# Kernel optimization log

Hardware: AMD Instinct MI355X
Metric: run time of the kernel (lower is better)

## Reference

```python
import jax, jax.numpy as jnp
import numpy as np

N_NODES = 50000
N_EDGES = 800000
NDIM_IN = 64
EDIM = 64
NDIM_OUT = [128, 128]


def setup_inputs() -> dict:
    key = jax.random.key(0)
    ks = jax.random.split(key, 12)
    inp = {
        "nfeats": jax.random.normal(ks[0], (N_NODES, 1, NDIM_IN), dtype=jnp.float32),
        "efeats": jax.random.normal(ks[1], (N_EDGES, 1, EDIM), dtype=jnp.float32),
        "dst": jax.random.randint(ks[2], (N_EDGES,), 0, N_NODES, dtype=jnp.int32),
    }
    # Layer 0 MLP: Linear(ndim_in+edim -> 128), ReLU, Linear(128 -> 128), ReLU
    d0_in = NDIM_IN + EDIM
    s = 1.0 / np.sqrt(d0_in)
    inp["W1_0"] = jax.random.uniform(ks[3], (d0_in, NDIM_OUT[0]), jnp.float32, -s, s)
    inp["b1_0"] = jax.random.uniform(ks[4], (NDIM_OUT[0],), jnp.float32, -s, s)
    s = 1.0 / np.sqrt(NDIM_OUT[0])
    inp["W2_0"] = jax.random.uniform(ks[5], (NDIM_OUT[0], NDIM_OUT[0]), jnp.float32, -s, s)
    inp["b2_0"] = jax.random.uniform(ks[6], (NDIM_OUT[0],), jnp.float32, -s, s)
    # Layer 1 MLP: Linear(128+edim -> 128), ReLU, Linear(128 -> 128), ReLU
    d1_in = NDIM_OUT[0] + EDIM
    s = 1.0 / np.sqrt(d1_in)
    inp["W1_1"] = jax.random.uniform(ks[7], (d1_in, NDIM_OUT[1]), jnp.float32, -s, s)
    inp["b1_1"] = jax.random.uniform(ks[8], (NDIM_OUT[1],), jnp.float32, -s, s)
    s = 1.0 / np.sqrt(NDIM_OUT[1])
    inp["W2_1"] = jax.random.uniform(ks[9], (NDIM_OUT[1], NDIM_OUT[1]), jnp.float32, -s, s)
    inp["b2_1"] = jax.random.uniform(ks[10], (NDIM_OUT[1],), jnp.float32, -s, s)
    return inp


def _gin_layer(h, h_neigh, W1, b1, W2, b2):
    # concat node state with scatter-summed edge features, then 2-layer MLP
    x = jnp.concatenate([h, h_neigh], axis=-1)  # [N, 1, d_in + edim]
    x = jax.nn.relu(x @ W1 + b1)
    return jax.nn.relu(x @ W2 + b2)


def reference(nfeats, efeats, dst,
              W1_0, b1_0, W2_0, b2_0,
              W1_1, b1_1, W2_1, b2_1):
    n = nfeats.shape[0]
    # update_all(copy_e, sum): scatter-add edge features onto destination nodes.
    # efeats never changes (edge_update path disabled), so h_neigh is layer-invariant.
    h_neigh = jax.ops.segment_sum(efeats, dst, num_segments=n)  # [N, 1, edim]
    h = _gin_layer(nfeats, h_neigh, W1_0, b1_0, W2_0, b2_0)
    # dropout is identity in eval mode (deterministic reference)
    h = _gin_layer(h, h_neigh, W1_1, b1_1, W2_1, b2_1)
    return h.sum(axis=1)  # [N, ndim_out[-1]]
```

## Files before the change

kernel.cpp:

```cpp
#include <hip/hip_runtime.h>
#include <hip/hip_bf16.h>

#define N_NODES 50000
#define N_EDGES 800000
#define EDIM 64
#define NT 64
#define XS 200
#define N_TILES 49

typedef __attribute__((ext_vector_type(8))) short  bf16x8_t;
typedef __attribute__((ext_vector_type(4))) short  bf16x4_t;
typedef __attribute__((ext_vector_type(4))) float  f32x4_t;

__device__ __forceinline__ unsigned short f2bf(float f) {
    unsigned u = __float_as_uint(f);
    unsigned r = u + 0x7fff + ((u >> 16) & 1);
    return (unsigned short)(r >> 16);
}
__device__ __forceinline__ float bf2f(unsigned short s) {
    return __uint_as_float(((unsigned)s) << 16);
}

__global__ __launch_bounds__(256) void prep_w_kernel(
    const float* __restrict__ W1_0, const float* __restrict__ W2_0,
    const float* __restrict__ W1_1, const float* __restrict__ W2_1,
    unsigned short* __restrict__ wbuf)
{
    int bid = blockIdx.x, t = threadIdx.x;
    const float* W; unsigned short *whi, *wlo; int K, idx;
    if (bid < 64)       { W = W1_0; K = 128; whi = wbuf;          wlo = wbuf + 16384;  idx = bid * 256 + t; }
    else if (bid < 128) { W = W2_0; K = 128; whi = wbuf + 32768;  wlo = wbuf + 49152;  idx = (bid - 64) * 256 + t; }
    else if (bid < 224) { W = W1_1; K = 192; whi = wbuf + 65536;  wlo = wbuf + 90112;  idx = (bid - 128) * 256 + t; }
    else                { W = W2_1; K = 128; whi = wbuf + 114688; wlo = wbuf + 131072; idx = (bid - 224) * 256 + t; }
    int k = idx >> 7, n = idx & 127;
    float w = W[idx];
    unsigned short h = f2bf(w);
    unsigned short l = f2bf(w - bf2f(h));
    whi[n * K + k] = h;
    wlo[n * K + k] = l;
}


__global__ __launch_bounds__(256) void hist_kernel(const int* __restrict__ dst,
                                                   int* __restrict__ cnt)
{
    int i = blockIdx.x * 256 + threadIdx.x;
    if (i < N_EDGES / 4) {
        int4 d = ((const int4*)dst)[i];
        atomicAdd(&cnt[d.x], 1);
        atomicAdd(&cnt[d.y], 1);
        atomicAdd(&cnt[d.z], 1);
        atomicAdd(&cnt[d.w], 1);
    }
}

__global__ __launch_bounds__(1024) void scan_reduce_kernel(const int* __restrict__ cnt,
                                                           int* __restrict__ btot)
{
    __shared__ int wsum[16];
    int t = threadIdx.x, lane = t & 63, w = t >> 6;
    int i = blockIdx.x * 1024 + t;
    int v = (i < N_NODES) ? cnt[i] : 0;
    #pragma unroll
    for (int off = 32; off > 0; off >>= 1) v += __shfl_xor(v, off);
    if (lane == 0) wsum[w] = v;
    __syncthreads();
    if (w == 0) {
        int s = (lane < 16) ? wsum[lane] : 0;
        #pragma unroll
        for (int off = 32; off > 0; off >>= 1) s += __shfl_xor(s, off);
        if (lane == 0) btot[blockIdx.x] = s;
    }
}

__global__ __launch_bounds__(1024) void scan_apply_kernel(int* __restrict__ cnt,
                                                          const int* __restrict__ btot)
{
    __shared__ int wsum[16];
    __shared__ int base_s;
    int t = threadIdx.x, lane = t & 63, w = t >> 6;

    if (t < 64) {
        int v = (t < N_TILES) ? btot[t] : 0;
        int x = v;
        #pragma unroll
        for (int off = 1; off < 64; off <<= 1) {
            int u = __shfl_up(x, off);
            if (lane >= off) x += u;
        }
        if (t == blockIdx.x) base_s = x - v;
    }

    int i = blockIdx.x * 1024 + t;
    int v = (i < N_NODES) ? cnt[i] : 0;
    int x = v;
    #pragma unroll
    for (int off = 1; off < 64; off <<= 1) {
        int u = __shfl_up(x, off);
        if (lane >= off) x += u;
    }
    if (lane == 63) wsum[w] = x;
    __syncthreads();
    if (w == 0) {
        int s = (lane < 16) ? wsum[lane] : 0;
        #pragma unroll
        for (int off = 1; off < 16; off <<= 1) {
            int u = __shfl_up(s, off);
            if (lane >= off) s += u;
        }
        if (lane < 16) wsum[lane] = s;
    }
    __syncthreads();
    int base = base_s + ((w == 0) ? 0 : wsum[w - 1]);
    if (i < N_NODES) cnt[i] = base + (x - v);
}

__global__ __launch_bounds__(256) void reorder_kernel(const int* __restrict__ dst,
                                                      int* __restrict__ offs,
                                                      int* __restrict__ order)
{
    int i = blockIdx.x * 256 + threadIdx.x;
    if (i < N_EDGES / 4) {
        int4 d = ((const int4*)dst)[i];
        int e0 = i * 4;
        int p0 = atomicAdd(&offs[d.x], 1);
        int p1 = atomicAdd(&offs[d.y], 1);
        int p2 = atomicAdd(&offs[d.z], 1);
        int p3 = atomicAdd(&offs[d.w], 1);
        order[p0] = e0;
        order[p1] = e0 + 1;
        order[p2] = e0 + 2;
        order[p3] = e0 + 3;
    }
}

__global__ __launch_bounds__(256) void gather_kernel(const float* __restrict__ ef,
                                                     const int* __restrict__ offs,
                                                     const int* __restrict__ order,
                                                     float* __restrict__ hn)
{
    int node = blockIdx.x * 4 + (threadIdx.x >> 6);
    int lane = threadIdx.x & 63;
    if (node >= N_NODES) return;
    int s = (node == 0) ? 0 : offs[node - 1];
    int e = offs[node];
    float a[8];
    #pragma unroll
    for (int k = 0; k < 8; ++k) a[k] = 0.f;

    int j = s;
    for (; j + 8 <= e; j += 8) {
        int idx[8];
        #pragma unroll
        for (int k = 0; k < 8; ++k) idx[k] = order[j + k];
        #pragma unroll
        for (int k = 0; k < 8; ++k)
            a[k] += __builtin_nontemporal_load(ef + (size_t)idx[k] * 64 + lane);
    }
    for (; j < e; ++j)
        a[0] += __builtin_nontemporal_load(ef + (size_t)order[j] * 64 + lane);

    float r = ((a[0] + a[1]) + (a[2] + a[3])) + ((a[4] + a[5]) + (a[6] + a[7]));
    hn[(size_t)node * 64 + lane] = r;
}


__device__ __forceinline__ void stage_x(short* Xhi, short* Xlo,
                                        const float* __restrict__ g,
                                        int node0, int k0, int t)
{
    #pragma unroll
    for (int rep = 0; rep < 4; ++rep) {
        int idx  = rep * 256 + t;
        int node = idx >> 4;
        int kq   = idx & 15;
        int gn   = node0 + node;
        float4 v = make_float4(0.f, 0.f, 0.f, 0.f);
        if (gn < N_NODES) v = *(const float4*)(g + (size_t)gn * 64 + kq * 4);
        unsigned short h0 = f2bf(v.x), h1 = f2bf(v.y), h2 = f2bf(v.z), h3 = f2bf(v.w);
        bf16x4_t hv = {(short)h0, (short)h1, (short)h2, (short)h3};
        bf16x4_t lv = {(short)f2bf(v.x - bf2f(h0)), (short)f2bf(v.y - bf2f(h1)),
                       (short)f2bf(v.z - bf2f(h2)), (short)f2bf(v.w - bf2f(h3))};
        *(bf16x4_t*)(&Xhi[node * XS + k0 + kq * 4]) = hv;
        *(bf16x4_t*)(&Xlo[node * XS + k0 + kq * 4]) = lv;
    }
}

template <int KTOT, bool FINAL>
__device__ __forceinline__ void mfma_linear(short* Xhi, short* Xlo,
    const unsigned short* __restrict__ whi, const unsigned short* __restrict__ wlo,
    const float* __restrict__ bias, float* __restrict__ out, int node0, int t)
{
    const int lane = t & 63, wv = t >> 6, quad = lane >> 4, l15 = lane & 15;
    const int chb = wv * 32;

    f32x4_t acc[4][2];
    #pragma unroll
    for (int mt = 0; mt < 4; ++mt) {
        acc[mt][0] = (f32x4_t){0.f, 0.f, 0.f, 0.f};
        acc[mt][1] = (f32x4_t){0.f, 0.f, 0.f, 0.f};
    }
    float bv0 = bias[chb + l15];
    float bv1 = bias[chb + 16 + l15];

    const unsigned short* w0h = whi + (size_t)(chb + l15) * KTOT;
    const unsigned short* w0l = wlo + (size_t)(chb + l15) * KTOT;
    const unsigned short* w1h = whi + (size_t)(chb + 16 + l15) * KTOT;
    const unsigned short* w1l = wlo + (size_t)(chb + 16 + l15) * KTOT;

    #pragma unroll
    for (int ks = 0; ks < KTOT / 32; ++ks) {
        int kk = ks * 32 + quad * 8;
        bf16x8_t b0h = *(const bf16x8_t*)(w0h + kk);
        bf16x8_t b0l = *(const bf16x8_t*)(w0l + kk);
        bf16x8_t b1h = *(const bf16x8_t*)(w1h + kk);
        bf16x8_t b1l = *(const bf16x8_t*)(w1l + kk);
        #pragma unroll
        for (int mt = 0; mt < 4; ++mt) {
            bf16x8_t ah = *(const bf16x8_t*)(&Xhi[(mt * 16 + l15) * XS + kk]);
            bf16x8_t al = *(const bf16x8_t*)(&Xlo[(mt * 16 + l15) * XS + kk]);
            acc[mt][0] = __builtin_amdgcn_mfma_f32_16x16x32_bf16(ah, b0h, acc[mt][0], 0, 0, 0);
            acc[mt][0] = __builtin_amdgcn_mfma_f32_16x16x32_bf16(al, b0h, acc[mt][0], 0, 0, 0);
            acc[mt][0] = __builtin_amdgcn_mfma_f32_16x16x32_bf16(ah, b0l, acc[mt][0], 0, 0, 0);
            acc[mt][1] = __builtin_amdgcn_mfma_f32_16x16x32_bf16(ah, b1h, acc[mt][1], 0, 0, 0);
            acc[mt][1] = __builtin_amdgcn_mfma_f32_16x16x32_bf16(al, b1h, acc[mt][1], 0, 0, 0);
            acc[mt][1] = __builtin_amdgcn_mfma_f32_16x16x32_bf16(ah, b1l, acc[mt][1], 0, 0, 0);
        }
    }

    __syncthreads();

    if (!FINAL) {
        #pragma unroll
        for (int mt = 0; mt < 4; ++mt) {
            #pragma unroll
            for (int nt = 0; nt < 2; ++nt) {
                float bb = nt ? bv1 : bv0;
                int ch = chb + nt * 16 + l15;
                #pragma unroll
                for (int r = 0; r < 4; ++r) {
                    float y = fmaxf(acc[mt][nt][r] + bb, 0.f);
                    unsigned short h = f2bf(y);
                    unsigned short l = f2bf(y - bf2f(h));
                    int m = mt * 16 + quad * 4 + r;
                    Xhi[m * XS + ch] = (short)h;
                    Xlo[m * XS + ch] = (short)l;
                }
            }
        }
        __syncthreads();
    } else {
        #pragma unroll
        for (int mt = 0; mt < 4; ++mt) {
            #pragma unroll
            for (int nt = 0; nt < 2; ++nt) {
                float bb = nt ? bv1 : bv0;
                int ch = chb + nt * 16 + l15;
                #pragma unroll
                for (int r = 0; r < 4; ++r) {
                    int gn = node0 + mt * 16 + quad * 4 + r;
                    if (gn < N_NODES)
                        out[(size_t)gn * 128 + ch] = fmaxf(acc[mt][nt][r] + bb, 0.f);
                }
            }
        }
    }
}

__global__ __launch_bounds__(256) void gin_mlp_mfma_kernel(
    const float* __restrict__ nfeats, const float* __restrict__ hneigh,
    const unsigned short* __restrict__ wbuf,
    const float* __restrict__ b1_0, const float* __restrict__ b2_0,
    const float* __restrict__ b1_1, const float* __restrict__ b2_1,
    float* __restrict__ out)
{
    __shared__ short Xhi[NT * XS];
    __shared__ short Xlo[NT * XS];
    const int t = threadIdx.x;
    const int node0 = blockIdx.x * NT;

    stage_x(Xhi, Xlo, nfeats, node0, 0, t);
    stage_x(Xhi, Xlo, hneigh, node0, 64, t);
    stage_x(Xhi, Xlo, hneigh, node0, 128, t);
    __syncthreads();

    mfma_linear<128, false>(Xhi, Xlo, wbuf,          wbuf + 16384,  b1_0, nullptr, node0, t);
    mfma_linear<128, false>(Xhi, Xlo, wbuf + 32768,  wbuf + 49152,  b2_0, nullptr, node0, t);
    mfma_linear<192, false>(Xhi, Xlo, wbuf + 65536,  wbuf + 90112,  b1_1, nullptr, node0, t);
    mfma_linear<128, true >(Xhi, Xlo, wbuf + 114688, wbuf + 131072, b2_1, out,     node0, t);
}

extern "C" void kernel_launch(void* const* d_in, const int* in_sizes, int n_in,
                              void* d_out, int out_size, void* d_ws, size_t ws_size,
                              hipStream_t stream)
{
    const float* nfeats = (const float*)d_in[0];
    const float* efeats = (const float*)d_in[1];
    const int*   dst    = (const int*)d_in[2];
    const float* W1_0   = (const float*)d_in[3];
    const float* b1_0   = (const float*)d_in[4];
    const float* W2_0   = (const float*)d_in[5];
    const float* b2_0   = (const float*)d_in[6];
    const float* W1_1   = (const float*)d_in[7];
    const float* b1_1   = (const float*)d_in[8];
    const float* W2_1   = (const float*)d_in[9];
    const float* b2_1   = (const float*)d_in[10];
    float* out = (float*)d_out;

    char* ws = (char*)d_ws;
    float*          hneigh = (float*)ws;
    int*            offs   = (int*)(ws + 12800000);
    int*            order  = (int*)(ws + 13000192);
    int*            btot   = (int*)(ws + 16200192);
    unsigned short* wbuf   = (unsigned short*)(ws + 16200448);

    hipMemsetAsync(offs, 0, N_NODES * sizeof(int), stream);

    prep_w_kernel<<<288, 256, 0, stream>>>(W1_0, W2_0, W1_1, W2_1, wbuf);

    hist_kernel<<<(N_EDGES / 4 + 255) / 256, 256, 0, stream>>>(dst, offs);
    scan_reduce_kernel<<<N_TILES, 1024, 0, stream>>>(offs, btot);
    scan_apply_kernel<<<N_TILES, 1024, 0, stream>>>(offs, btot);
    reorder_kernel<<<(N_EDGES / 4 + 255) / 256, 256, 0, stream>>>(dst, offs, order);
    gather_kernel<<<(N_NODES + 3) / 4, 256, 0, stream>>>(efeats, offs, order, hneigh);

    int nblk = (N_NODES + NT - 1) / NT;
    gin_mlp_mfma_kernel<<<nblk, 256, 0, stream>>>(
        nfeats, hneigh, wbuf, b1_0, b2_0, b1_1, b2_1, out);
}
```

Measured before the change: 451.1 us.

## Fuse edge-feature gather into the MLP kernel, writing sums directly to LDS

```diff
diff --git a/kernel.cpp b/kernel.cpp
--- a/kernel.cpp
+++ b/kernel.cpp
@@ -132,36 +132,6 @@
         order[p2] = e0 + 2;
         order[p3] = e0 + 3;
     }
-}
-
-__global__ __launch_bounds__(256) void gather_kernel(const float* __restrict__ ef,
-                                                     const int* __restrict__ offs,
-                                                     const int* __restrict__ order,
-                                                     float* __restrict__ hn)
-{
-    int node = blockIdx.x * 4 + (threadIdx.x >> 6);
-    int lane = threadIdx.x & 63;
-    if (node >= N_NODES) return;
-    int s = (node == 0) ? 0 : offs[node - 1];
-    int e = offs[node];
-    float a[8];
-    #pragma unroll
-    for (int k = 0; k < 8; ++k) a[k] = 0.f;
-
-    int j = s;
-    for (; j + 8 <= e; j += 8) {
-        int idx[8];
-        #pragma unroll
-        for (int k = 0; k < 8; ++k) idx[k] = order[j + k];
-        #pragma unroll
-        for (int k = 0; k < 8; ++k)
-            a[k] += __builtin_nontemporal_load(ef + (size_t)idx[k] * 64 + lane);
-    }
-    for (; j < e; ++j)
-        a[0] += __builtin_nontemporal_load(ef + (size_t)order[j] * 64 + lane);
-
-    float r = ((a[0] + a[1]) + (a[2] + a[3])) + ((a[4] + a[5]) + (a[6] + a[7]));
-    hn[(size_t)node * 64 + lane] = r;
 }
 
 
@@ -267,8 +237,9 @@
     }
 }
 
-__global__ __launch_bounds__(256) void gin_mlp_mfma_kernel(
-    const float* __restrict__ nfeats, const float* __restrict__ hneigh,
+__global__ __launch_bounds__(256) void gin_fused_kernel(
+    const float* __restrict__ nfeats, const float* __restrict__ efeats,
+    const int* __restrict__ offs, const int* __restrict__ order,
     const unsigned short* __restrict__ wbuf,
     const float* __restrict__ b1_0, const float* __restrict__ b2_0,
     const float* __restrict__ b1_1, const float* __restrict__ b2_1,
@@ -278,10 +249,46 @@
     __shared__ short Xlo[NT * XS];
     const int t = threadIdx.x;
     const int node0 = blockIdx.x * NT;
+    const int wv = t >> 6, lane = t & 63;
+
+    const int nb = node0 + wv * 16;
+    int bo = 0;
+    if (lane <= 16) {
+        int ii = nb - 1 + lane;
+        if (ii >= N_NODES) ii = N_NODES - 1;
+        bo = (ii < 0) ? 0 : offs[ii];
+    }
 
     stage_x(Xhi, Xlo, nfeats, node0, 0, t);
-    stage_x(Xhi, Xlo, hneigh, node0, 64, t);
-    stage_x(Xhi, Xlo, hneigh, node0, 128, t);
+
+    for (int i = 0; i < 16; ++i) {
+        int s = __builtin_amdgcn_readfirstlane(__shfl(bo, i));
+        int e = __builtin_amdgcn_readfirstlane(__shfl(bo, i + 1));
+        float a[8];
+        #pragma unroll
+        for (int k = 0; k < 8; ++k) a[k] = 0.f;
+
+        int j = s;
+        for (; j + 8 <= e; j += 8) {
+            int idx[8];
+            #pragma unroll
+            for (int k = 0; k < 8; ++k) idx[k] = order[j + k];
+            #pragma unroll
+            for (int k = 0; k < 8; ++k)
+                a[k] += __builtin_nontemporal_load(efeats + (size_t)idx[k] * 64 + lane);
+        }
+        for (; j < e; ++j)
+            a[0] += __builtin_nontemporal_load(efeats + (size_t)order[j] * 64 + lane);
+
+        float r = ((a[0] + a[1]) + (a[2] + a[3])) + ((a[4] + a[5]) + (a[6] + a[7]));
+        unsigned short h = f2bf(r);
+        unsigned short l = f2bf(r - bf2f(h));
+        int row = (wv * 16 + i) * XS;
+        Xhi[row + 64  + lane] = (short)h;
+        Xhi[row + 128 + lane] = (short)h;
+        Xlo[row + 64  + lane] = (short)l;
+        Xlo[row + 128 + lane] = (short)l;
+    }
     __syncthreads();
 
     mfma_linear<128, false>(Xhi, Xlo, wbuf,          wbuf + 16384,  b1_0, nullptr, node0, t);
@@ -308,11 +315,10 @@
     float* out = (float*)d_out;
 
     char* ws = (char*)d_ws;
-    float*          hneigh = (float*)ws;
-    int*            offs   = (int*)(ws + 12800000);
-    int*            order  = (int*)(ws + 13000192);
-    int*            btot   = (int*)(ws + 16200192);
-    unsigned short* wbuf   = (unsigned short*)(ws + 16200448);
+    int*            offs  = (int*)ws;
+    int*            order = (int*)(ws + 200704);
+    int*            btot  = (int*)(ws + 3400704);
+    unsigned short* wbuf  = (unsigned short*)(ws + 3400960);
 
     hipMemsetAsync(offs, 0, N_NODES * sizeof(int), stream);
 
@@ -322,9 +328,8 @@
     scan_reduce_kernel<<<N_TILES, 1024, 0, stream>>>(offs, btot);
     scan_apply_kernel<<<N_TILES, 1024, 0, stream>>>(offs, btot);
     reorder_kernel<<<(N_EDGES / 4 + 255) / 256, 256, 0, stream>>>(dst, offs, order);
-    gather_kernel<<<(N_NODES + 3) / 4, 256, 0, stream>>>(efeats, offs, order, hneigh);
 
     int nblk = (N_NODES + NT - 1) / NT;
-    gin_mlp_mfma_kernel<<<nblk, 256, 0, stream>>>(
-        nfeats, hneigh, wbuf, b1_0, b2_0, b1_1, b2_1, out);
-}
+    gin_fused_kernel<<<nblk, 256, 0, stream>>>(
+        nfeats, efeats, offs, order, wbuf, b1_0, b2_0, b1_1, b2_1, out);
+}
```

New measurement: 492.3 us. 1.09x slower.

## Replace CSR sort-and-gather with fixed-point integer atomic scatter-add

Applied to the files above, without the earlier changes.

```diff
diff --git a/kernel.cpp b/kernel.cpp
--- a/kernel.cpp
+++ b/kernel.cpp
@@ -6,7 +6,9 @@
 #define EDIM 64
 #define NT 64
 #define XS 200
-#define N_TILES 49
+
+#define FP_SCALE 2097152.0f
+#define FP_INV   (1.0f / 2097152.0f)
 
 typedef __attribute__((ext_vector_type(8))) short  bf16x8_t;
 typedef __attribute__((ext_vector_type(4))) short  bf16x4_t;
@@ -40,128 +42,23 @@
     wlo[n * K + k] = l;
 }
 
-
-__global__ __launch_bounds__(256) void hist_kernel(const int* __restrict__ dst,
-                                                   int* __restrict__ cnt)
-{
-    int i = blockIdx.x * 256 + threadIdx.x;
-    if (i < N_EDGES / 4) {
-        int4 d = ((const int4*)dst)[i];
-        atomicAdd(&cnt[d.x], 1);
-        atomicAdd(&cnt[d.y], 1);
-        atomicAdd(&cnt[d.z], 1);
-        atomicAdd(&cnt[d.w], 1);
-    }
-}
-
-__global__ __launch_bounds__(1024) void scan_reduce_kernel(const int* __restrict__ cnt,
-                                                           int* __restrict__ btot)
-{
-    __shared__ int wsum[16];
-    int t = threadIdx.x, lane = t & 63, w = t >> 6;
-    int i = blockIdx.x * 1024 + t;
-    int v = (i < N_NODES) ? cnt[i] : 0;
-    #pragma unroll
-    for (int off = 32; off > 0; off >>= 1) v += __shfl_xor(v, off);
-    if (lane == 0) wsum[w] = v;
-    __syncthreads();
-    if (w == 0) {
-        int s = (lane < 16) ? wsum[lane] : 0;
-        #pragma unroll
-        for (int off = 32; off > 0; off >>= 1) s += __shfl_xor(s, off);
-        if (lane == 0) btot[blockIdx.x] = s;
-    }
-}
-
-__global__ __launch_bounds__(1024) void scan_apply_kernel(int* __restrict__ cnt,
-                                                          const int* __restrict__ btot)
-{
-    __shared__ int wsum[16];
-    __shared__ int base_s;
-    int t = threadIdx.x, lane = t & 63, w = t >> 6;
-
-    if (t < 64) {
-        int v = (t < N_TILES) ? btot[t] : 0;
-        int x = v;
-        #pragma unroll
-        for (int off = 1; off < 64; off <<= 1) {
-            int u = __shfl_up(x, off);
-            if (lane >= off) x += u;
-        }
-        if (t == blockIdx.x) base_s = x - v;
-    }
-
-    int i = blockIdx.x * 1024 + t;
-    int v = (i < N_NODES) ? cnt[i] : 0;
-    int x = v;
-    #pragma unroll
-    for (int off = 1; off < 64; off <<= 1) {
-        int u = __shfl_up(x, off);
-        if (lane >= off) x += u;
-    }
-    if (lane == 63) wsum[w] = x;
-    __syncthreads();
-    if (w == 0) {
-        int s = (lane < 16) ? wsum[lane] : 0;
-        #pragma unroll
-        for (int off = 1; off < 16; off <<= 1) {
-            int u = __shfl_up(s, off);
-            if (lane >= off) s += u;
-        }
-        if (lane < 16) wsum[lane] = s;
-    }
-    __syncthreads();
-    int base = base_s + ((w == 0) ? 0 : wsum[w - 1]);
-    if (i < N_NODES) cnt[i] = base + (x - v);
-}
-
-__global__ __launch_bounds__(256) void reorder_kernel(const int* __restrict__ dst,
-                                                      int* __restrict__ offs,
-                                                      int* __restrict__ order)
-{
-    int i = blockIdx.x * 256 + threadIdx.x;
-    if (i < N_EDGES / 4) {
-        int4 d = ((const int4*)dst)[i];
-        int e0 = i * 4;
-        int p0 = atomicAdd(&offs[d.x], 1);
-        int p1 = atomicAdd(&offs[d.y], 1);
-        int p2 = atomicAdd(&offs[d.z], 1);
-        int p3 = atomicAdd(&offs[d.w], 1);
-        order[p0] = e0;
-        order[p1] = e0 + 1;
-        order[p2] = e0 + 2;
-        order[p3] = e0 + 3;
-    }
-}
-
-__global__ __launch_bounds__(256) void gather_kernel(const float* __restrict__ ef,
-                                                     const int* __restrict__ offs,
-                                                     const int* __restrict__ order,
-                                                     float* __restrict__ hn)
-{
-    int node = blockIdx.x * 4 + (threadIdx.x >> 6);
-    int lane = threadIdx.x & 63;
-    if (node >= N_NODES) return;
-    int s = (node == 0) ? 0 : offs[node - 1];
-    int e = offs[node];
-    float a[8];
-    #pragma unroll
-    for (int k = 0; k < 8; ++k) a[k] = 0.f;
-
-    int j = s;
-    for (; j + 8 <= e; j += 8) {
-        int idx[8];
-        #pragma unroll
-        for (int k = 0; k < 8; ++k) idx[k] = order[j + k];
-        #pragma unroll
-        for (int k = 0; k < 8; ++k)
-            a[k] += __builtin_nontemporal_load(ef + (size_t)idx[k] * 64 + lane);
-    }
-    for (; j < e; ++j)
-        a[0] += __builtin_nontemporal_load(ef + (size_t)order[j] * 64 + lane);
-
-    float r = ((a[0] + a[1]) + (a[2] + a[3])) + ((a[4] + a[5]) + (a[6] + a[7]));
-    hn[(size_t)node * 64 + lane] = r;
+__global__ __launch_bounds__(256) void scatter_kernel(const float* __restrict__ ef,
+                                                      const int* __restrict__ dst,
+                                                      int* __restrict__ hn)
+{
+    const int NITEM = N_EDGES * 16;
+    const int stride = gridDim.x * 256;
+    for (int i = blockIdx.x * 256 + threadIdx.x; i < NITEM; i += stride) {
+        int e  = i >> 4;
+        int c4 = (i & 15) << 2;
+        float4 v = ((const float4*)ef)[i];
+        int d = dst[e];
+        int* p = hn + (size_t)d * 64 + c4;
+        atomicAdd(p + 0, __float2int_rn(v.x * FP_SCALE));
+        atomicAdd(p + 1, __float2int_rn(v.y * FP_SCALE));
+        atomicAdd(p + 2, __float2int_rn(v.z * FP_SCALE));
+        atomicAdd(p + 3, __float2int_rn(v.w * FP_SCALE));
+    }
 }
 
 
@@ -183,6 +80,34 @@
                        (short)f2bf(v.z - bf2f(h2)), (short)f2bf(v.w - bf2f(h3))};
         *(bf16x4_t*)(&Xhi[node * XS + k0 + kq * 4]) = hv;
         *(bf16x4_t*)(&Xlo[node * XS + k0 + kq * 4]) = lv;
+    }
+}
+
+__device__ __forceinline__ void stage_hn(short* Xhi, short* Xlo,
+                                         const int* __restrict__ g,
+                                         int node0, int t)
+{
+    #pragma unroll
+    for (int rep = 0; rep < 4; ++rep) {
+        int idx  = rep * 256 + t;
+        int node = idx >> 4;
+        int kq   = idx & 15;
+        int gn   = node0 + node;
+        float4 v = make_float4(0.f, 0.f, 0.f, 0.f);
+        if (gn < N_NODES) {
+            int4 iv = *(const int4*)(g + (size_t)gn * 64 + kq * 4);
+            v = make_float4(iv.x * FP_INV, iv.y * FP_INV, iv.z * FP_INV, iv.w * FP_INV);
+        }
+        unsigned short h0 = f2bf(v.x), h1 = f2bf(v.y), h2 = f2bf(v.z), h3 = f2bf(v.w);
+        bf16x4_t hv = {(short)h0, (short)h1, (short)h2, (short)h3};
+        bf16x4_t lv = {(short)f2bf(v.x - bf2f(h0)), (short)f2bf(v.y - bf2f(h1)),
+                       (short)f2bf(v.z - bf2f(h2)), (short)f2bf(v.w - bf2f(h3))};
+        int r0 = node * XS + 64 + kq * 4;
+        int r1 = node * XS + 128 + kq * 4;
+        *(bf16x4_t*)(&Xhi[r0]) = hv;
+        *(bf16x4_t*)(&Xlo[r0]) = lv;
+        *(bf16x4_t*)(&Xhi[r1]) = hv;
+        *(bf16x4_t*)(&Xlo[r1]) = lv;
     }
 }
 
@@ -268,7 +193,7 @@
 }
 
 __global__ __launch_bounds__(256) void gin_mlp_mfma_kernel(
-    const float* __restrict__ nfeats, const float* __restrict__ hneigh,
+    const float* __restrict__ nfeats, const int* __restrict__ hn_int,
     const unsigned short* __restrict__ wbuf,
     const float* __restrict__ b1_0, const float* __restrict__ b2_0,
     const float* __restrict__ b1_1, const float* __restrict__ b2_1,
@@ -280,8 +205,7 @@
     const int node0 = blockIdx.x * NT;
 
     stage_x(Xhi, Xlo, nfeats, node0, 0, t);
-    stage_x(Xhi, Xlo, hneigh, node0, 64, t);
-    stage_x(Xhi, Xlo, hneigh, node0, 128, t);
+    stage_hn(Xhi, Xlo, hn_int, node0, t);
     __syncthreads();
 
     mfma_linear<128, false>(Xhi, Xlo, wbuf,          wbuf + 16384,  b1_0, nullptr, node0, t);
@@ -308,23 +232,16 @@
     float* out = (float*)d_out;
 
     char* ws = (char*)d_ws;
-    float*          hneigh = (float*)ws;
-    int*            offs   = (int*)(ws + 12800000);
-    int*            order  = (int*)(ws + 13000192);
-    int*            btot   = (int*)(ws + 16200192);
-    unsigned short* wbuf   = (unsigned short*)(ws + 16200448);
-
-    hipMemsetAsync(offs, 0, N_NODES * sizeof(int), stream);
+    int*            hn_int = (int*)ws;
+    unsigned short* wbuf   = (unsigned short*)(ws + 12800000);
 
     prep_w_kernel<<<288, 256, 0, stream>>>(W1_0, W2_0, W1_1, W2_1, wbuf);
 
-    hist_kernel<<<(N_EDGES / 4 + 255) / 256, 256, 0, stream>>>(dst, offs);
-    scan_reduce_kernel<<<N_TILES, 1024, 0, stream>>>(offs, btot);
-    scan_apply_kernel<<<N_TILES, 1024, 0, stream>>>(offs, btot);
-    reorder_kernel<<<(N_EDGES / 4 + 255) / 256, 256, 0, stream>>>(dst, offs, order);
-    gather_kernel<<<(N_NODES + 3) / 4, 256, 0, stream>>>(efeats, offs, order, hneigh);
+    hipMemsetAsync(hn_int, 0, N_NODES * 64 * sizeof(int), stream);
+
+    scatter_kernel<<<2048, 256, 0, stream>>>(efeats, dst, hn_int);
 
     int nblk = (N_NODES + NT - 1) / NT;
     gin_mlp_mfma_kernel<<<nblk, 256, 0, stream>>>(
-        nfeats, hneigh, wbuf, b1_0, b2_0, b1_1, b2_1, out);
-}
+        nfeats, hn_int, wbuf, b1_0, b2_0, b1_1, b2_1, out);
+}
```

Result: slower. 823.4 us (+82.5%).
